# Optimization experiments

Measured on AMD Instinct MI355X. Metric: run time of the kernel, lower is better.

The kernel has to match this reference:

```python
import jax, jax.numpy as jnp
import numpy as np

HEADS = 4
DIM_HEAD = 32
CHUNK = 1024
GROUPS = 8
EPS = 1e-5


def setup_inputs() -> dict:
    key = jax.random.key(0)
    k1, k2, k3 = jax.random.split(key, 3)
    b, dim, h, w = 8, 64, 96, 96
    inner = HEADS * DIM_HEAD  # 128
    x = jax.random.normal(k1, (b, dim, h, w), dtype=jnp.float32)
    W_qkv = jax.random.normal(k2, (3 * inner, dim), dtype=jnp.float32) * (1.0 / np.sqrt(dim))
    W_out = jax.random.normal(k3, (dim, inner), dtype=jnp.float32) * (1.0 / np.sqrt(inner))
    b_out = jnp.zeros((dim,), dtype=jnp.float32)
    gamma = jnp.ones((dim,), dtype=jnp.float32)
    beta = jnp.zeros((dim,), dtype=jnp.float32)
    return {"x": x, "W_qkv": W_qkv, "W_out": W_out, "b_out": b_out,
            "gamma": gamma, "beta": beta}


def reference(x, W_qkv, W_out, b_out, gamma, beta):
    b, c, h, w = x.shape
    n = h * w
    nch = n // CHUNK  # number of full chunks (n chosen divisible by CHUNK)
    d = DIM_HEAD
    BH = b * HEADS

    # 1x1 conv (no bias) == matmul over channel dim
    xf = x.reshape(b, c, n)
    qkv = jnp.einsum('oc,bcn->bon', W_qkv, xf)          # [b, 3*inner, n]
    q, k, v = jnp.split(qkv, 3, axis=1)                  # each [b, inner, n]

    def chunkify(t):
        # [b, inner, n] -> [BH, nch, d, CHUNK]; slicing i:i+CHUNK on last axis
        # equals reshaping n -> (nch, CHUNK) in order.
        return t.reshape(BH, d, nch, CHUNK).transpose(0, 2, 1, 3)

    qc, kc, vc = chunkify(q), chunkify(k), chunkify(v)

    qs = jax.nn.softmax(qc, axis=-1)  # softmax over chunk spatial positions
    ks = jax.nn.softmax(kc, axis=-2)  # softmax over head channels

    # context = k_chunk^T @ v_chunk : [BH, nch, CHUNK, CHUNK]
    ctx = jnp.einsum('gkdi,gkdj->gkij', ks, vc)
    # chunk_out = q_chunk @ context : [BH, nch, d, CHUNK]
    out = jnp.einsum('gkdi,gkij->gkdj', qs, ctx)

    # concat chunks back along spatial dim, reshape to image layout
    out = out.transpose(0, 2, 1, 3).reshape(b, HEADS * d, h, w)

    # to_out: 1x1 conv with bias, then GroupNorm(8, dim)
    y = jnp.einsum('oc,bchw->bohw', W_out, out) + b_out[None, :, None, None]

    yg = y.reshape(b, GROUPS, c // GROUPS, h, w)
    mu = jnp.mean(yg, axis=(2, 3, 4), keepdims=True)
    var = jnp.var(yg, axis=(2, 3, 4), keepdims=True)
    yn = ((yg - mu) * jax.lax.rsqrt(var + EPS)).reshape(b, c, h, w)
    return yn * gamma[None, :, None, None] + beta[None, :, None, None]
```

## Files before the change

### kernel.cpp

```cpp
#include <hip/hip_runtime.h>
#include <hip/hip_bf16.h>

#define N_POS 9216
#define NCHUNK 9
#define BATCH 8
#define CDIM 64
#define HEADS 4
#define EPS 1e-5f

#define NPART 16
#define PPARTS_TOT ((size_t)BATCH * NCHUNK * NPART * 4096)
#define MP_SLICE ((size_t)(BATCH * NCHUNK) * 4096)
#define WBF_BYTES ((size_t)384 * 64 * 2)

typedef __attribute__((ext_vector_type(8))) short short8;
typedef __attribute__((ext_vector_type(4))) float f32x4;

static __device__ inline unsigned pk2(float a, float b) {
    __hip_bfloat162 h2(__float2bfloat16(a), __float2bfloat16(b));
    return *reinterpret_cast<unsigned*>(&h2);
}
static __device__ inline float bf2f(short s) {
    union { unsigned u; float f; } c; c.u = ((unsigned)(unsigned short)s) << 16; return c.f;
}

__global__ __launch_bounds__(256) void wprep_kernel(const float* __restrict__ Wqkv,
        __hip_bfloat16* __restrict__ wbf, float* __restrict__ stats) {
    int i = blockIdx.x * 256 + threadIdx.x;
    if (i < 6144) {
        float4 v = ((const float4*)Wqkv)[i];
        uint2 u; u.x = pk2(v.x, v.y); u.y = pk2(v.z, v.w);
        ((uint2*)wbf)[i] = u;
    }
    if (i < 128) stats[i] = 0.f;
}

__global__ __launch_bounds__(256) void qkp_kernel(const float* __restrict__ x,
        const __hip_bfloat16* __restrict__ wbf, float* __restrict__ Pparts) {
    int bx = blockIdx.x;
    int b  = blockIdx.y;
    int ck = bx >> 4, pt = bx & 15;
    __shared__ __align__(16) __hip_bfloat16 xs[64][72];
    __shared__ __align__(16) __hip_bfloat16 skT[256][72];
    int t = threadIdx.x, w = t >> 6, l = t & 63;
    int l15 = l & 15, quad = l >> 4;
    int n0 = bx * 64;

    {
        int p = t & 63, cbase = (t >> 6) * 16;
        const float* xb = x + (size_t)b * CDIM * N_POS + n0 + p;
        #pragma unroll
        for (int j = 0; j < 16; j += 4) {
            float v0 = xb[(size_t)(cbase + j + 0) * N_POS];
            float v1 = xb[(size_t)(cbase + j + 1) * N_POS];
            float v2 = xb[(size_t)(cbase + j + 2) * N_POS];
            float v3 = xb[(size_t)(cbase + j + 3) * N_POS];
            uint2 u; u.x = pk2(v0, v1); u.y = pk2(v2, v3);
            *reinterpret_cast<uint2*>(&xs[p][cbase + j]) = u;
        }
    }
    __syncthreads();

    f32x4 acc[4][4];
    #pragma unroll
    for (int mt = 0; mt < 4; ++mt)
        #pragma unroll
        for (int nt = 0; nt < 4; ++nt) acc[mt][nt] = (f32x4){0.f, 0.f, 0.f, 0.f};
    #pragma unroll
    for (int ks = 0; ks < 2; ++ks) {
        int k0 = ks * 32 + quad * 8;
        short8 av[4];
        #pragma unroll
        for (int mt = 0; mt < 4; ++mt)
            av[mt] = *reinterpret_cast<const short8*>(&xs[mt * 16 + l15][k0]);
        #pragma unroll
        for (int nt = 0; nt < 4; ++nt) {
            short8 bw = *reinterpret_cast<const short8*>(wbf + (size_t)(w * 64 + nt * 16 + l15) * 64 + k0);
            #pragma unroll
            for (int mt = 0; mt < 4; ++mt)
                acc[mt][nt] = __builtin_amdgcn_mfma_f32_16x16x32_bf16(av[mt], bw, acc[mt][nt], 0, 0, 0);
        }
    }

    if (w < 2) {
        #pragma unroll
        for (int nt = 0; nt < 4; ++nt) {
            int ch = w * 64 + nt * 16 + l15;
            #pragma unroll
            for (int mt = 0; mt < 4; ++mt) {
                uint2 u;
                u.x = pk2(__expf(acc[mt][nt][0]), __expf(acc[mt][nt][1]));
                u.y = pk2(__expf(acc[mt][nt][2]), __expf(acc[mt][nt][3]));
                *reinterpret_cast<uint2*>(&skT[ch][mt * 16 + quad * 4]) = u;
            }
        }
    } else {
        #pragma unroll
        for (int hh = 0; hh < 2; ++hh) {
            int h = (w - 2) * 2 + hh;
            #pragma unroll
            for (int mt = 0; mt < 4; ++mt) {
                f32x4 a0 = acc[mt][2 * hh], a1 = acc[mt][2 * hh + 1];
                f32x4 e0, e1;
                #pragma unroll
                for (int r = 0; r < 4; ++r) {
                    float m = fmaxf(a0[r], a1[r]);
                    m = fmaxf(m, __shfl_xor(m, 1));
                    m = fmaxf(m, __shfl_xor(m, 2));
                    m = fmaxf(m, __shfl_xor(m, 4));
                    m = fmaxf(m, __shfl_xor(m, 8));
                    float x0 = __expf(a0[r] - m), x1 = __expf(a1[r] - m);
                    float s = x0 + x1;
                    s += __shfl_xor(s, 1);
                    s += __shfl_xor(s, 2);
                    s += __shfl_xor(s, 4);
                    s += __shfl_xor(s, 8);
                    float is = 1.f / s;
                    e0[r] = x0 * is; e1[r] = x1 * is;
                }
                uint2 u;
                u.x = pk2(e0[0], e0[1]); u.y = pk2(e0[2], e0[3]);
                *reinterpret_cast<uint2*>(&skT[128 + h * 32 + l15][mt * 16 + quad * 4]) = u;
                u.x = pk2(e1[0], e1[1]); u.y = pk2(e1[2], e1[3]);
                *reinterpret_cast<uint2*>(&skT[128 + h * 32 + 16 + l15][mt * 16 + quad * 4]) = u;
            }
        }
    }
    __syncthreads();

    f32x4 pac[2][2];
    pac[0][0] = (f32x4){0,0,0,0}; pac[0][1] = (f32x4){0,0,0,0};
    pac[1][0] = (f32x4){0,0,0,0}; pac[1][1] = (f32x4){0,0,0,0};
    #pragma unroll
    for (int ks = 0; ks < 2; ++ks) {
        int k0 = ks * 32 + quad * 8;
        short8 aq0 = *reinterpret_cast<const short8*>(&skT[w * 32 + l15][k0]);
        short8 aq1 = *reinterpret_cast<const short8*>(&skT[w * 32 + 16 + l15][k0]);
        short8 bk0 = *reinterpret_cast<const short8*>(&skT[128 + w * 32 + l15][k0]);
        short8 bk1 = *reinterpret_cast<const short8*>(&skT[128 + w * 32 + 16 + l15][k0]);
        pac[0][0] = __builtin_amdgcn_mfma_f32_16x16x32_bf16(aq0, bk0, pac[0][0], 0, 0, 0);
        pac[0][1] = __builtin_amdgcn_mfma_f32_16x16x32_bf16(aq0, bk1, pac[0][1], 0, 0, 0);
        pac[1][0] = __builtin_amdgcn_mfma_f32_16x16x32_bf16(aq1, bk0, pac[1][0], 0, 0, 0);
        pac[1][1] = __builtin_amdgcn_mfma_f32_16x16x32_bf16(aq1, bk1, pac[1][1], 0, 0, 0);
    }
    float* Pp = Pparts + (((size_t)(b * NCHUNK + ck) * NPART + pt) * 4 + w) * 1024;
    #pragma unroll
    for (int tA = 0; tA < 2; ++tA)
        #pragma unroll
        for (int tB = 0; tB < 2; ++tB)
            #pragma unroll
            for (int r = 0; r < 4; ++r)
                Pp[(tA * 16 + quad * 4 + r) * 32 + tB * 16 + l15] = pac[tA][tB][r];
}

__global__ __launch_bounds__(256) void umat_kernel(const float* __restrict__ Wout,
        const float* __restrict__ Wqkv, const float* __restrict__ Pparts,
        float* __restrict__ Mp) {
    int ck = blockIdx.x, b = blockIdx.y, h = blockIdx.z;
    int t = threadIdx.x;
    __shared__ float Pl[32][32];
    __shared__ float iZ[32];
    __shared__ float Ul[64][33];
    __shared__ float Wvh[32][68];
    {
        const float4* P0 = (const float4*)Pparts
            + ((size_t)(b * NCHUNK + ck) * NPART) * 1024 + h * 256 + t;
        float4 s = (float4){0.f, 0.f, 0.f, 0.f};
        #pragma unroll
        for (int pt = 0; pt < NPART; ++pt) {
            float4 a = P0[pt * 1024];
            s.x += a.x; s.y += a.y; s.z += a.z; s.w += a.w;
        }
        ((float4*)Pl)[t] = s;
    }
    {
        int e = t >> 3, cq = t & 7;
        const float4* wr = (const float4*)(Wqkv + (size_t)(256 + h * 32 + e) * 64 + cq * 8);
        float4 a0 = wr[0], a1 = wr[1];
        *reinterpret_cast<float4*>(&Wvh[e][cq * 8])     = a0;
        *reinterpret_cast<float4*>(&Wvh[e][cq * 8 + 4]) = a1;
    }
    __syncthreads();
    if (t < 32) {
        float s = 0.f;
        #pragma unroll
        for (int c = 0; c < 32; ++c) s += Pl[t][c];
        iZ[t] = 1.f / s;
    }
    __syncthreads();
    int o = t & 63, wv = t >> 6;
    float wz[32];
    {
        const float4* wr = (const float4*)(Wout + (size_t)o * 128 + h * 32);
        #pragma unroll
        for (int j = 0; j < 8; ++j) {
            float4 f = wr[j];
            wz[j*4+0] = f.x * iZ[j*4+0]; wz[j*4+1] = f.y * iZ[j*4+1];
            wz[j*4+2] = f.z * iZ[j*4+2]; wz[j*4+3] = f.w * iZ[j*4+3];
        }
    }
    float ua[8];
    #pragma unroll
    for (int j = 0; j < 8; ++j) ua[j] = 0.f;
    for (int d = 0; d < 32; ++d) {
        float wd = wz[d];
        #pragma unroll
        for (int j = 0; j < 8; ++j) ua[j] += wd * Pl[d][wv * 8 + j];
    }
    #pragma unroll
    for (int j = 0; j < 8; ++j) Ul[o][wv * 8 + j] = ua[j];
    __syncthreads();

    float macc[16];
    #pragma unroll
    for (int j = 0; j < 16; ++j) macc[j] = 0.f;
    for (int e = 0; e < 32; ++e) {
        float u = Ul[o][e];
        const float4* wvp = reinterpret_cast<const float4*>(&Wvh[e][wv * 16]);
        #pragma unroll
        for (int q = 0; q < 4; ++q) {
            float4 f = wvp[q];
            macc[q*4+0] += u * f.x; macc[q*4+1] += u * f.y;
            macc[q*4+2] += u * f.z; macc[q*4+3] += u * f.w;
        }
    }
    float* mp = Mp + (size_t)h * MP_SLICE + ((size_t)(b * NCHUNK + ck)) * 4096
              + (size_t)o * 64 + wv * 16;
    #pragma unroll
    for (int q = 0; q < 4; ++q) {
        float4 f; f.x = macc[q*4+0]; f.y = macc[q*4+1]; f.z = macc[q*4+2]; f.w = macc[q*4+3];
        reinterpret_cast<float4*>(mp)[q] = f;
    }
}

__global__ __launch_bounds__(256) void y_kernel(const float* __restrict__ x,
        const float* __restrict__ Mp, const float* __restrict__ bout,
        __hip_bfloat16* __restrict__ ybf, float* __restrict__ stats) {
    int bx = blockIdx.x;
    int b  = blockIdx.y;
    int ck = bx >> 3;
    int n0 = bx * 128;
    __shared__ __align__(16) __hip_bfloat16 xs[128][72];
    __shared__ __align__(16) __hip_bfloat16 Ml[64][72];
    __shared__ float gsum[8], gsq[8];
    int t = threadIdx.x, w = t >> 6, l = t & 63;
    int l15 = l & 15, quad = l >> 4;
    if (t < 8) { gsum[t] = 0.f; gsq[t] = 0.f; }

    {
        int p = t & 127, cbase = (t >> 7) * 32;
        const float* xb = x + (size_t)b * CDIM * N_POS + n0 + p;
        #pragma unroll
        for (int j = 0; j < 32; j += 4) {
            float v0 = xb[(size_t)(cbase + j + 0) * N_POS];
            float v1 = xb[(size_t)(cbase + j + 1) * N_POS];
            float v2 = xb[(size_t)(cbase + j + 2) * N_POS];
            float v3 = xb[(size_t)(cbase + j + 3) * N_POS];
            uint2 u; u.x = pk2(v0, v1); u.y = pk2(v2, v3);
            *reinterpret_cast<uint2*>(&xs[p][cbase + j]) = u;
        }
    }
    {
        int o = t >> 2, cs = (t & 3) * 16;
        const float* mb = Mp + ((size_t)(b * NCHUNK + ck)) * 4096 + (size_t)o * 64 + cs;
        float m[16];
        #pragma unroll
        for (int q = 0; q < 4; ++q) {
            float4 f = reinterpret_cast<const float4*>(mb)[q];
            m[q*4+0] = f.x; m[q*4+1] = f.y; m[q*4+2] = f.z; m[q*4+3] = f.w;
        }
        #pragma unroll
        for (int h = 1; h < 4; ++h) {
            const float* mh = mb + h * MP_SLICE;
            #pragma unroll
            for (int q = 0; q < 4; ++q) {
                float4 f = reinterpret_cast<const float4*>(mh)[q];
                m[q*4+0] += f.x; m[q*4+1] += f.y; m[q*4+2] += f.z; m[q*4+3] += f.w;
            }
        }
        #pragma unroll
        for (int q = 0; q < 4; ++q) {
            uint2 u; u.x = pk2(m[q*4+0], m[q*4+1]); u.y = pk2(m[q*4+2], m[q*4+3]);
            *reinterpret_cast<uint2*>(&Ml[o][cs + q * 4]) = u;
        }
    }
    __syncthreads();

    int nw = w * 32;
    f32x4 acc[4][2];
    #pragma unroll
    for (int mt = 0; mt < 4; ++mt) { acc[mt][0] = (f32x4){0,0,0,0}; acc[mt][1] = (f32x4){0,0,0,0}; }
    #pragma unroll
    for (int ks = 0; ks < 2; ++ks) {
        int k0 = ks * 32 + quad * 8;
        short8 bf[2];
        #pragma unroll
        for (int nt = 0; nt < 2; ++nt)
            bf[nt] = *reinterpret_cast<const short8*>(&xs[nw + nt * 16 + l15][k0]);
        #pragma unroll
        for (int mt = 0; mt < 4; ++mt) {
            short8 af = *reinterpret_cast<const short8*>(&Ml[mt * 16 + l15][k0]);
            acc[mt][0] = __builtin_amdgcn_mfma_f32_16x16x32_bf16(af, bf[0], acc[mt][0], 0, 0, 0);
            acc[mt][1] = __builtin_amdgcn_mfma_f32_16x16x32_bf16(af, bf[1], acc[mt][1], 0, 0, 0);
        }
    }
    float gsl[4], gql[4];
    #pragma unroll
    for (int mt = 0; mt < 4; ++mt) { gsl[mt] = 0.f; gql[mt] = 0.f; }
    __hip_bfloat16* yb = ybf + (size_t)b * CDIM * N_POS;
    int nbase = n0 + nw;
    #pragma unroll
    for (int mt = 0; mt < 4; ++mt) {
        float4 bo = *reinterpret_cast<const float4*>(bout + mt * 16 + quad * 4);
        const float* bop = reinterpret_cast<const float*>(&bo);
        #pragma unroll
        for (int nt = 0; nt < 2; ++nt) {
            int n = nbase + nt * 16 + l15;
            #pragma unroll
            for (int r = 0; r < 4; ++r) {
                int o = mt * 16 + quad * 4 + r;
                float val = acc[mt][nt][r] + bop[r];
                yb[(size_t)o * N_POS + n] = __float2bfloat16(val);
                gsl[mt] += val; gql[mt] += val * val;
            }
        }
    }
    #pragma unroll
    for (int off = 16; off >= 1; off >>= 1) {
        #pragma unroll
        for (int mt = 0; mt < 4; ++mt) {
            gsl[mt] += __shfl_xor(gsl[mt], off, 64);
            gql[mt] += __shfl_xor(gql[mt], off, 64);
        }
    }
    if (l == 0 || l == 32) {
        int qh = quad >> 1;
        #pragma unroll
        for (int mt = 0; mt < 4; ++mt) {
            atomicAdd(&gsum[2 * mt + qh], gsl[mt]);
            atomicAdd(&gsq[2 * mt + qh], gql[mt]);
        }
    }
    __syncthreads();
    if (t < 8) {
        atomicAdd(&stats[(b * 8 + t) * 2],     gsum[t]);
        atomicAdd(&stats[(b * 8 + t) * 2 + 1], gsq[t]);
    }
}

__global__ __launch_bounds__(256) void gn_kernel(const __hip_bfloat16* __restrict__ ybf,
        float* __restrict__ out, const float* __restrict__ stats,
        const float* __restrict__ gamma, const float* __restrict__ beta) {
    int bc = blockIdx.y;
    int c = bc & 63, b = bc >> 6;
    int g = c >> 3;
    float s = stats[(b * 8 + g) * 2], q = stats[(b * 8 + g) * 2 + 1];
    const float invN = 1.f / (8.f * N_POS);
    float mean = s * invN;
    float var = q * invN - mean * mean;
    float sc = rsqrtf(var + EPS);
    float ga = gamma[c] * sc;
    float be = beta[c] - mean * sc * gamma[c];
    size_t base = ((size_t)b * CDIM + c) * N_POS + (size_t)(blockIdx.x * 256 + threadIdx.x) * 4;
    uint2 u = *reinterpret_cast<const uint2*>(ybf + base);
    float4 v;
    v.x = bf2f((short)(u.x & 0xffff)); v.y = bf2f((short)(u.x >> 16));
    v.z = bf2f((short)(u.y & 0xffff)); v.w = bf2f((short)(u.y >> 16));
    v.x = v.x * ga + be; v.y = v.y * ga + be; v.z = v.z * ga + be; v.w = v.w * ga + be;
    *reinterpret_cast<float4*>(out + base) = v;
}

extern "C" void kernel_launch(void* const* d_in, const int* in_sizes, int n_in,
                              void* d_out, int out_size, void* d_ws, size_t ws_size,
                              hipStream_t stream) {
    const float* x     = (const float*)d_in[0];
    const float* Wqkv  = (const float*)d_in[1];
    const float* Wout  = (const float*)d_in[2];
    const float* bout  = (const float*)d_in[3];
    const float* gamma = (const float*)d_in[4];
    const float* beta  = (const float*)d_in[5];
    float* out = (float*)d_out;

    float* stats  = (float*)d_ws;
    float* Pparts = stats + 128;
    float* Mp     = Pparts + PPARTS_TOT;
    __hip_bfloat16* wbf = (__hip_bfloat16*)(Mp + 4 * MP_SLICE);
    __hip_bfloat16* ybf = (__hip_bfloat16*)((char*)wbf + WBF_BYTES);

    wprep_kernel<<<dim3(24), 256, 0, stream>>>(Wqkv, wbf, stats);
    qkp_kernel<<<dim3(144, BATCH), 256, 0, stream>>>(x, wbf, Pparts);
    umat_kernel<<<dim3(NCHUNK, BATCH, HEADS), 256, 0, stream>>>(Wout, Wqkv, Pparts, Mp);
    y_kernel<<<dim3(72, BATCH), 256, 0, stream>>>(x, Mp, bout, ybf, stats);
    gn_kernel<<<dim3(9, 512), 256, 0, stream>>>(ybf, out, stats, gamma, beta);
}
```

Before: 132.7 us.

## Keep softmaxed q/k fragments in registers via lane shuffles instead of LDS

Each wave now computes the q and k channels for its own head, so the per-head q·k products no longer need other waves' data. The exp/softmax results are packed to bf16 in registers and rearranged into MFMA operand layout with cross-lane shuffles. This removes the large skT shared-memory buffer, its stores and loads, and a block barrier, which also frees LDS for occupancy. In exchange it issues many ds_bpermute shuffles and more register pressure, and every wave now runs the softmax shuffle reductions where before only two of the four waves did.

```diff
diff --git a/kernel.cpp b/kernel.cpp
--- a/kernel.cpp
+++ b/kernel.cpp
@@ -22,6 +22,10 @@
 }
 static __device__ inline float bf2f(short s) {
     union { unsigned u; float f; } c; c.u = ((unsigned)(unsigned short)s) << 16; return c.f;
+}
+static __device__ inline short8 mk8(unsigned a, unsigned b, unsigned c, unsigned d) {
+    union { short8 s; unsigned u[4]; } cv;
+    cv.u[0] = a; cv.u[1] = b; cv.u[2] = c; cv.u[3] = d; return cv.s;
 }
 
 __global__ __launch_bounds__(256) void wprep_kernel(const float* __restrict__ Wqkv,
@@ -41,7 +45,6 @@
     int b  = blockIdx.y;
     int ck = bx >> 4, pt = bx & 15;
     __shared__ __align__(16) __hip_bfloat16 xs[64][72];
-    __shared__ __align__(16) __hip_bfloat16 skT[256][72];
     int t = threadIdx.x, w = t >> 6, l = t & 63;
     int l15 = l & 15, quad = l >> 4;
     int n0 = bx * 64;
@@ -75,73 +78,70 @@
             av[mt] = *reinterpret_cast<const short8*>(&xs[mt * 16 + l15][k0]);
         #pragma unroll
         for (int nt = 0; nt < 4; ++nt) {
-            short8 bw = *reinterpret_cast<const short8*>(wbf + (size_t)(w * 64 + nt * 16 + l15) * 64 + k0);
+            int row = (nt < 2) ? (w * 32 + nt * 16 + l15)
+                               : (128 + w * 32 + (nt - 2) * 16 + l15);
+            short8 bw = *reinterpret_cast<const short8*>(wbf + (size_t)row * 64 + k0);
             #pragma unroll
             for (int mt = 0; mt < 4; ++mt)
                 acc[mt][nt] = __builtin_amdgcn_mfma_f32_16x16x32_bf16(av[mt], bw, acc[mt][nt], 0, 0, 0);
         }
     }
 
-    if (w < 2) {
-        #pragma unroll
-        for (int nt = 0; nt < 4; ++nt) {
-            int ch = w * 64 + nt * 16 + l15;
-            #pragma unroll
-            for (int mt = 0; mt < 4; ++mt) {
-                uint2 u;
-                u.x = pk2(__expf(acc[mt][nt][0]), __expf(acc[mt][nt][1]));
-                u.y = pk2(__expf(acc[mt][nt][2]), __expf(acc[mt][nt][3]));
-                *reinterpret_cast<uint2*>(&skT[ch][mt * 16 + quad * 4]) = u;
-            }
-        }
-    } else {
-        #pragma unroll
-        for (int hh = 0; hh < 2; ++hh) {
-            int h = (w - 2) * 2 + hh;
-            #pragma unroll
-            for (int mt = 0; mt < 4; ++mt) {
-                f32x4 a0 = acc[mt][2 * hh], a1 = acc[mt][2 * hh + 1];
-                f32x4 e0, e1;
-                #pragma unroll
-                for (int r = 0; r < 4; ++r) {
-                    float m = fmaxf(a0[r], a1[r]);
-                    m = fmaxf(m, __shfl_xor(m, 1));
-                    m = fmaxf(m, __shfl_xor(m, 2));
-                    m = fmaxf(m, __shfl_xor(m, 4));
-                    m = fmaxf(m, __shfl_xor(m, 8));
-                    float x0 = __expf(a0[r] - m), x1 = __expf(a1[r] - m);
-                    float s = x0 + x1;
-                    s += __shfl_xor(s, 1);
-                    s += __shfl_xor(s, 2);
-                    s += __shfl_xor(s, 4);
-                    s += __shfl_xor(s, 8);
-                    float is = 1.f / s;
-                    e0[r] = x0 * is; e1[r] = x1 * is;
-                }
-                uint2 u;
-                u.x = pk2(e0[0], e0[1]); u.y = pk2(e0[2], e0[3]);
-                *reinterpret_cast<uint2*>(&skT[128 + h * 32 + l15][mt * 16 + quad * 4]) = u;
-                u.x = pk2(e1[0], e1[1]); u.y = pk2(e1[2], e1[3]);
-                *reinterpret_cast<uint2*>(&skT[128 + h * 32 + 16 + l15][mt * 16 + quad * 4]) = u;
-            }
-        }
-    }
-    __syncthreads();
+    unsigned pk[4][4][2];
+    #pragma unroll
+    for (int mt = 0; mt < 4; ++mt) {
+        f32x4 e2, e3;
+        #pragma unroll
+        for (int r = 0; r < 4; ++r) {
+            float a2 = acc[mt][2][r], a3 = acc[mt][3][r];
+            float m = fmaxf(a2, a3);
+            m = fmaxf(m, __shfl_xor(m, 1));
+            m = fmaxf(m, __shfl_xor(m, 2));
+            m = fmaxf(m, __shfl_xor(m, 4));
+            m = fmaxf(m, __shfl_xor(m, 8));
+            float x2 = __expf(a2 - m), x3 = __expf(a3 - m);
+            float s = x2 + x3;
+            s += __shfl_xor(s, 1);
+            s += __shfl_xor(s, 2);
+            s += __shfl_xor(s, 4);
+            s += __shfl_xor(s, 8);
+            float is = 1.f / s;
+            e2[r] = x2 * is; e3[r] = x3 * is;
+        }
+        pk[mt][2][0] = pk2(e2[0], e2[1]); pk[mt][2][1] = pk2(e2[2], e2[3]);
+        pk[mt][3][0] = pk2(e3[0], e3[1]); pk[mt][3][1] = pk2(e3[2], e3[3]);
+        pk[mt][0][0] = pk2(__expf(acc[mt][0][0]), __expf(acc[mt][0][1]));
+        pk[mt][0][1] = pk2(__expf(acc[mt][0][2]), __expf(acc[mt][0][3]));
+        pk[mt][1][0] = pk2(__expf(acc[mt][1][0]), __expf(acc[mt][1][1]));
+        pk[mt][1][1] = pk2(__expf(acc[mt][1][2]), __expf(acc[mt][1][3]));
+    }
 
     f32x4 pac[2][2];
     pac[0][0] = (f32x4){0,0,0,0}; pac[0][1] = (f32x4){0,0,0,0};
     pac[1][0] = (f32x4){0,0,0,0}; pac[1][1] = (f32x4){0,0,0,0};
+    int srcbase = ((quad & 1) * 2) * 16 + l15;
+    bool hiHalf = (quad >= 2);
     #pragma unroll
     for (int ks = 0; ks < 2; ++ks) {
-        int k0 = ks * 32 + quad * 8;
-        short8 aq0 = *reinterpret_cast<const short8*>(&skT[w * 32 + l15][k0]);
-        short8 aq1 = *reinterpret_cast<const short8*>(&skT[w * 32 + 16 + l15][k0]);
-        short8 bk0 = *reinterpret_cast<const short8*>(&skT[128 + w * 32 + l15][k0]);
-        short8 bk1 = *reinterpret_cast<const short8*>(&skT[128 + w * 32 + 16 + l15][k0]);
-        pac[0][0] = __builtin_amdgcn_mfma_f32_16x16x32_bf16(aq0, bk0, pac[0][0], 0, 0, 0);
-        pac[0][1] = __builtin_amdgcn_mfma_f32_16x16x32_bf16(aq0, bk1, pac[0][1], 0, 0, 0);
-        pac[1][0] = __builtin_amdgcn_mfma_f32_16x16x32_bf16(aq1, bk0, pac[1][0], 0, 0, 0);
-        pac[1][1] = __builtin_amdgcn_mfma_f32_16x16x32_bf16(aq1, bk1, pac[1][1], 0, 0, 0);
+        unsigned fr[4][4];
+        #pragma unroll
+        for (int nt = 0; nt < 4; ++nt) {
+            #pragma unroll
+            for (int s = 0; s < 4; ++s) {
+                int src = srcbase + (s >> 1) * 16;
+                unsigned lo = __shfl(pk[2 * ks][nt][s & 1], src);
+                unsigned hi = __shfl(pk[2 * ks + 1][nt][s & 1], src);
+                fr[nt][s] = hiHalf ? hi : lo;
+            }
+        }
+        short8 A0 = mk8(fr[0][0], fr[0][1], fr[0][2], fr[0][3]);
+        short8 A1 = mk8(fr[1][0], fr[1][1], fr[1][2], fr[1][3]);
+        short8 B0 = mk8(fr[2][0], fr[2][1], fr[2][2], fr[2][3]);
+        short8 B1 = mk8(fr[3][0], fr[3][1], fr[3][2], fr[3][3]);
+        pac[0][0] = __builtin_amdgcn_mfma_f32_16x16x32_bf16(A0, B0, pac[0][0], 0, 0, 0);
+        pac[0][1] = __builtin_amdgcn_mfma_f32_16x16x32_bf16(A0, B1, pac[0][1], 0, 0, 0);
+        pac[1][0] = __builtin_amdgcn_mfma_f32_16x16x32_bf16(A1, B0, pac[1][0], 0, 0, 0);
+        pac[1][1] = __builtin_amdgcn_mfma_f32_16x16x32_bf16(A1, B1, pac[1][1], 0, 0, 0);
     }
     float* Pp = Pparts + (((size_t)(b * NCHUNK + ck) * NPART + pt) * 4 + w) * 1024;
     #pragma unroll
```

Result: no change. 130.9 us (-1.4%).
